# Optimization experiments

Measured on AMD Instinct MI355X. Metric: run time of the kernel, lower is better.

The kernel has to match this reference:

```python
import jax, jax.numpy as jnp
import numpy as np

N = 100000      # nodes (cells)
E = 1600000     # edges (kNN graph, avg degree 16)
DIM_IN = 128    # input features per cell
H = 8           # heads
C1 = 8          # per-head channels, layer 1 (concat -> 64)
DIM_OUT = 10    # classes (concat=False -> mean over heads)
NEG_SLOPE = 0.2


def setup_inputs() -> dict:
    key = jax.random.key(0)
    ks = jax.random.split(key, 10)
    s = 0.1
    return {
        "x": jax.random.normal(ks[0], (N, DIM_IN), dtype=jnp.float32),
        "edge_index": jax.random.randint(ks[1], (2, E), 0, N, dtype=jnp.int64),
        "W1": jax.random.normal(ks[2], (DIM_IN, H * C1), dtype=jnp.float32) * s,
        "a_src1": jax.random.normal(ks[3], (H, C1), dtype=jnp.float32) * s,
        "a_dst1": jax.random.normal(ks[4], (H, C1), dtype=jnp.float32) * s,
        "b1": jnp.zeros((H * C1,), dtype=jnp.float32),
        "W2": jax.random.normal(ks[5], (H * C1, H * DIM_OUT), dtype=jnp.float32) * s,
        "a_src2": jax.random.normal(ks[6], (H, DIM_OUT), dtype=jnp.float32) * s,
        "a_dst2": jax.random.normal(ks[7], (H, DIM_OUT), dtype=jnp.float32) * s,
        "b2": jnp.zeros((DIM_OUT,), dtype=jnp.float32),
    }


def _gat_layer(x, src, dst, W, a_src, a_dst, bias, concat, n):
    """PyG-style GATConv: gather -> edge attention -> segment softmax -> scatter."""
    h_, c_ = a_src.shape
    h = (x @ W).reshape(n, h_, c_)                       # [N, H, C]
    alpha_s = jnp.einsum('nhc,hc->nh', h, a_src)         # [N, H]
    alpha_d = jnp.einsum('nhc,hc->nh', h, a_dst)         # [N, H]
    # per-edge logits; PyG: message from src j to dst i, softmax over dst
    e = jax.nn.leaky_relu(alpha_s[src] + alpha_d[dst], NEG_SLOPE)  # [E, H]
    e_max = jax.ops.segment_max(e, dst, num_segments=n)            # [N, H]
    e = jnp.exp(e - e_max[dst])
    denom = jax.ops.segment_sum(e, dst, num_segments=n)            # [N, H]
    alpha = e / denom[dst]                                          # [E, H]
    msg = h[src] * alpha[:, :, None]                                # [E, H, C]
    out = jax.ops.segment_sum(msg, dst, num_segments=n)             # [N, H, C]
    out = out.reshape(n, h_ * c_) if concat else out.mean(axis=1)
    return out + bias


def reference(x, edge_index, W1, a_src1, a_dst1, b1, W2, a_src2, a_dst2, b2):
    n = x.shape[0]
    loops = jnp.arange(n, dtype=edge_index.dtype)
    src = jnp.concatenate([edge_index[0], loops])  # PyG adds self-loops by default
    dst = jnp.concatenate([edge_index[1], loops])
    h = _gat_layer(x, src, dst, W1, a_src1, a_dst1, b1, True, n)   # [N, 64]
    h = jax.nn.elu(h)
    h = _gat_layer(h, src, dst, W2, a_src2, a_dst2, b2, False, n)  # [N, dim_out]
    return jax.nn.log_softmax(h, axis=1)
```

## Files before the change

kernel.cpp:

```cpp
#include <hip/hip_runtime.h>
#include <hip/hip_bf16.h>
#include <cstdint>

#define CAP 64
#define SLICES 8
#define CHUNK_EDGES 2048

__device__ __forceinline__ float lrelu(float v) { return fmaxf(v, 0.2f * v); }

typedef float f32x2 __attribute__((ext_vector_type(2)));
__device__ __forceinline__ float2 q2f(unsigned short u) {
    f32x2 v = __builtin_amdgcn_cvt_pk_f32_fp8((int)u, false);
    return make_float2(v.x, v.y);
}
__device__ __forceinline__ int f2q4(float a, float b, float c, float d) {
    int p = __builtin_amdgcn_cvt_pk_fp8_f32(a, b, 0, false);
    p = __builtin_amdgcn_cvt_pk_fp8_f32(c, d, p, true);
    return p;
}
__device__ __forceinline__ float b2f(unsigned short u) { return __uint_as_float(((unsigned)u) << 16); }
__device__ __forceinline__ unsigned short f2b(float f) {
    unsigned u = __float_as_uint(f);
    return (unsigned short)((u + 0x7FFFu + ((u >> 16) & 1u)) >> 16);
}

__global__ __launch_bounds__(256, 4) void k_bg(const int* __restrict__ ei, int E, int N,
                                               int* __restrict__ cnt, int* __restrict__ bucket,
                                               const float* __restrict__ x,
                                               const float* __restrict__ W,
                                               const float* __restrict__ asrc,
                                               const float* __restrict__ adst,
                                               unsigned char* __restrict__ h1q,
                                               float* __restrict__ als, float* __restrict__ ald,
                                               int buildBlocks) {
    __shared__ unsigned short xs[64 * 132];
    if ((int)blockIdx.x < buildBlocks) {
        const int s = blockIdx.x & (SLICES - 1);
        const int chunk = blockIdx.x >> 3;
        const int sliceN = (N + SLICES - 1) / SLICES;
        const int lo = s * sliceN;
        const int hi = min(N, lo + sliceN);
        const int base = chunk * CHUNK_EDGES;
        if (base + CHUNK_EDGES <= E) {
            const int e0 = base + (int)threadIdx.x * 4;
            const int e1 = e0 + 1024;
            int4 d0 = *(const int4*)(ei + E + e0);
            int4 s0 = *(const int4*)(ei + e0);
            int4 d1 = *(const int4*)(ei + E + e1);
            int4 s1 = *(const int4*)(ei + e1);
            int a0 = -1, a1 = -1, a2 = -1, a3 = -1, a4 = -1, a5 = -1, a6 = -1, a7 = -1;
            if (d0.x >= lo && d0.x < hi) a0 = atomicAdd(&cnt[d0.x], 1);
            if (d0.y >= lo && d0.y < hi) a1 = atomicAdd(&cnt[d0.y], 1);
            if (d0.z >= lo && d0.z < hi) a2 = atomicAdd(&cnt[d0.z], 1);
            if (d0.w >= lo && d0.w < hi) a3 = atomicAdd(&cnt[d0.w], 1);
            if (d1.x >= lo && d1.x < hi) a4 = atomicAdd(&cnt[d1.x], 1);
            if (d1.y >= lo && d1.y < hi) a5 = atomicAdd(&cnt[d1.y], 1);
            if (d1.z >= lo && d1.z < hi) a6 = atomicAdd(&cnt[d1.z], 1);
            if (d1.w >= lo && d1.w < hi) a7 = atomicAdd(&cnt[d1.w], 1);
            if (a0 >= 0 && a0 < CAP) bucket[(size_t)d0.x * CAP + a0] = s0.x;
            if (a1 >= 0 && a1 < CAP) bucket[(size_t)d0.y * CAP + a1] = s0.y;
            if (a2 >= 0 && a2 < CAP) bucket[(size_t)d0.z * CAP + a2] = s0.z;
            if (a3 >= 0 && a3 < CAP) bucket[(size_t)d0.w * CAP + a3] = s0.w;
            if (a4 >= 0 && a4 < CAP) bucket[(size_t)d1.x * CAP + a4] = s1.x;
            if (a5 >= 0 && a5 < CAP) bucket[(size_t)d1.y * CAP + a5] = s1.y;
            if (a6 >= 0 && a6 < CAP) bucket[(size_t)d1.z * CAP + a6] = s1.z;
            if (a7 >= 0 && a7 < CAP) bucket[(size_t)d1.w * CAP + a7] = s1.w;
        } else {
            const int end = E;
            for (int e = base + (int)threadIdx.x; e < end; e += 256) {
                int d = ei[E + e];
                if (d >= lo && d < hi) {
                    int a = atomicAdd(&cnt[d], 1);
                    if (a < CAP) bucket[(size_t)d * CAP + a] = ei[e];
                }
            }
        }
        return;
    }
    const int t = threadIdx.x;
    const int rowBase = ((int)blockIdx.x - buildBlocks) * 64;
#pragma unroll
    for (int i = 0; i < 8; ++i) {
        int g = i * 256 + t;
        int r = g >> 5, c4 = (g & 31) << 2;
        float4 v = make_float4(0.f, 0.f, 0.f, 0.f);
        int row = rowBase + r;
        if (row < N) v = *(const float4*)(x + (size_t)row * 128 + c4);
        ushort4 u;
        u.x = f2b(v.x); u.y = f2b(v.y); u.z = f2b(v.z); u.w = f2b(v.w);
        *(ushort4*)(&xs[r * 132 + c4]) = u;
    }
    __syncthreads();
    const int tx = t & 15;
    const int ty = t >> 4;
    float acc[4][4] = {};
#pragma unroll 2
    for (int kc = 0; kc < 32; ++kc) {
        float a_[4][4];
#pragma unroll
        for (int i = 0; i < 4; ++i) {
            ushort4 u = *(const ushort4*)(&xs[(4 * ty + i) * 132 + kc * 4]);
            a_[i][0] = b2f(u.x); a_[i][1] = b2f(u.y); a_[i][2] = b2f(u.z); a_[i][3] = b2f(u.w);
        }
        float4 w[4];
#pragma unroll
        for (int kk = 0; kk < 4; ++kk) w[kk] = *(const float4*)(W + (size_t)(kc * 4 + kk) * 64 + tx * 4);
#pragma unroll
        for (int i = 0; i < 4; ++i) {
#pragma unroll
            for (int j = 0; j < 4; ++j) {
                acc[i][j] += a_[i][0] * ((const float*)&w[0])[j]
                           + a_[i][1] * ((const float*)&w[1])[j]
                           + a_[i][2] * ((const float*)&w[2])[j]
                           + a_[i][3] * ((const float*)&w[3])[j];
            }
        }
    }
    const int h = tx >> 1;
    float4 av = *(const float4*)(asrc + tx * 4);
    float4 dv = *(const float4*)(adst + tx * 4);
#pragma unroll
    for (int i = 0; i < 4; ++i) {
        int row = rowBase + 4 * ty + i;
        float ps = acc[i][0] * av.x + acc[i][1] * av.y + acc[i][2] * av.z + acc[i][3] * av.w;
        float pd = acc[i][0] * dv.x + acc[i][1] * dv.y + acc[i][2] * dv.z + acc[i][3] * dv.w;
        ps += __shfl_xor(ps, 1);
        pd += __shfl_xor(pd, 1);
        if (row < N) {
            *(int*)(h1q + (size_t)row * 64 + tx * 4) = f2q4(acc[i][0], acc[i][1], acc[i][2], acc[i][3]);
            if ((tx & 1) == 0) {
                als[(size_t)row * 8 + h] = ps;
                ald[(size_t)row * 8 + h] = pd;
            }
        }
    }
}

__global__ __launch_bounds__(256) void k_gemm2(const float* __restrict__ hin,
                                               const float* __restrict__ W,
                                               const float* __restrict__ asrc,
                                               const float* __restrict__ adst,
                                               unsigned char* __restrict__ h2q,
                                               float* __restrict__ ald, int N) {
    __shared__ float xs[64 * 68];
    __shared__ float wt[80 * 68];
    const int t = threadIdx.x;
    const int rowBase = blockIdx.x * 64;
#pragma unroll
    for (int i = 0; i < 4; ++i) {
        int g = i * 256 + t;
        int r = g >> 4, c4 = (g & 15) << 2;
        float4 v = make_float4(0.f, 0.f, 0.f, 0.f);
        int row = rowBase + r;
        if (row < N) v = *(const float4*)(hin + (size_t)row * 64 + c4);
        *(float4*)(&xs[r * 68 + c4]) = v;
    }
#pragma unroll
    for (int i = 0; i < 20; ++i) {
        int g = i * 256 + t;
        int k = g / 80, c = g % 80;
        wt[c * 68 + k] = W[g];
    }
    __syncthreads();
    const int tx = t & 15;
    const int ty = t >> 4;
    float acc[4][5] = {};
#pragma unroll 4
    for (int kc = 0; kc < 16; ++kc) {
        float4 a[4];
#pragma unroll
        for (int i = 0; i < 4; ++i) a[i] = *(const float4*)(&xs[(4 * ty + i) * 68 + kc * 4]);
        float4 w[5];
#pragma unroll
        for (int j = 0; j < 5; ++j) w[j] = *(const float4*)(&wt[(5 * tx + j) * 68 + kc * 4]);
#pragma unroll
        for (int i = 0; i < 4; ++i) {
#pragma unroll
            for (int j = 0; j < 5; ++j) {
                acc[i][j] += a[i].x * w[j].x + a[i].y * w[j].y + a[i].z * w[j].z + a[i].w * w[j].w;
            }
        }
    }
    const int h = tx >> 1;
    float a2[5], d2[5];
#pragma unroll
    for (int j = 0; j < 5; ++j) { a2[j] = asrc[tx * 5 + j]; d2[j] = adst[tx * 5 + j]; }
    __syncthreads();
    unsigned char* qs = (unsigned char*)xs;
#pragma unroll
    for (int i = 0; i < 4; ++i) {
        int row = rowBase + 4 * ty + i;
        float ps = 0.f, pd = 0.f;
#pragma unroll
        for (int j = 0; j < 5; ++j) { ps += acc[i][j] * a2[j]; pd += acc[i][j] * d2[j]; }
        ps += __shfl_xor(ps, 1);
        pd += __shfl_xor(pd, 1);
        int p0 = __builtin_amdgcn_cvt_pk_fp8_f32(acc[i][0], acc[i][1], 0, false);
        int p1 = __builtin_amdgcn_cvt_pk_fp8_f32(acc[i][2], acc[i][3], 0, false);
        int p2 = __builtin_amdgcn_cvt_pk_fp8_f32(acc[i][4], acc[i][4], 0, false);
        unsigned char* q = qs + (4 * ty + i) * 96 + h * 12 + (tx & 1) * 5;
        q[0] = (unsigned char)(p0 & 0xFF);
        q[1] = (unsigned char)((p0 >> 8) & 0xFF);
        q[2] = (unsigned char)(p1 & 0xFF);
        q[3] = (unsigned char)((p1 >> 8) & 0xFF);
        q[4] = (unsigned char)(p2 & 0xFF);
        if ((tx & 1) == 0) {
            *(unsigned short*)(qs + (size_t)(4 * ty + i) * 96 + h * 12 + 10) = f2b(ps);
            if (row < N) ald[(size_t)row * 8 + h] = pd;
        }
    }
    __syncthreads();
    for (int g = t; g < 1536; g += 256) {
        int row = g / 24;
        if (rowBase + row < N)
            *(unsigned int*)(h2q + (size_t)rowBase * 96 + (size_t)g * 4) = ((unsigned int*)qs)[g];
    }
}

__global__ __launch_bounds__(256) void k_agg1(const int* __restrict__ cnt, const int* __restrict__ bucket,
                                              const unsigned char* __restrict__ h1q,
                                              const float* __restrict__ als, const float* __restrict__ ald,
                                              const float* __restrict__ b1,
                                              float* __restrict__ helu, int N) {
    const int t = threadIdx.x;
    const int n = blockIdx.x * 32 + (t >> 3);
    const int h = t & 7;
    if (n >= N) return;
    float acc[8] = {};
    float den = 0.f;
    const float aldh = ald[(size_t)n * 8 + h];
    auto body = [&](int m0, int m1, float a_s, float val) {
        float wl = __expf(lrelu(a_s + aldh)) * val;
        den += wl;
        f32x2 v;
        v = __builtin_amdgcn_cvt_pk_f32_fp8(m0, false); acc[0] += wl * v.x; acc[1] += wl * v.y;
        v = __builtin_amdgcn_cvt_pk_f32_fp8(m0, true);  acc[2] += wl * v.x; acc[3] += wl * v.y;
        v = __builtin_amdgcn_cvt_pk_f32_fp8(m1, false); acc[4] += wl * v.x; acc[5] += wl * v.y;
        v = __builtin_amdgcn_cvt_pk_f32_fp8(m1, true);  acc[6] += wl * v.x; acc[7] += wl * v.y;
    };
    {
        const unsigned char* r = h1q + (size_t)n * 64 + h * 8;
        body(*(const int*)r, *(const int*)(r + 4), als[(size_t)n * 8 + h], 1.f);
    }
    const int k = min(cnt[n], CAP);
    const int* bp = bucket + (size_t)n * CAP;
    if (k > 0) {
        const int kg = ((k - 1) >> 2) << 2;
        int4 nxt = *(const int4*)(bp);
        for (int i0 = 0; i0 < k; i0 += 4) {
            int4 cur = nxt;
            nxt = *(const int4*)(bp + min(i0 + 4, kg));
            const int rem = k - i0;
            const int s0 = cur.x;
            const int s1 = (rem > 1) ? cur.y : cur.x;
            const int s2 = (rem > 2) ? cur.z : cur.x;
            const int s3 = (rem > 3) ? cur.w : cur.x;
            const int2 r0 = *(const int2*)(h1q + (size_t)s0 * 64 + h * 8);
            const int2 r1 = *(const int2*)(h1q + (size_t)s1 * 64 + h * 8);
            const int2 r2 = *(const int2*)(h1q + (size_t)s2 * 64 + h * 8);
            const int2 r3 = *(const int2*)(h1q + (size_t)s3 * 64 + h * 8);
            const float a0 = als[(size_t)s0 * 8 + h];
            const float a1 = als[(size_t)s1 * 8 + h];
            const float a2 = als[(size_t)s2 * 8 + h];
            const float a3 = als[(size_t)s3 * 8 + h];
            body(r0.x, r0.y, a0, 1.f);
            body(r1.x, r1.y, a1, (rem > 1) ? 1.f : 0.f);
            body(r2.x, r2.y, a2, (rem > 2) ? 1.f : 0.f);
            body(r3.x, r3.y, a3, (rem > 3) ? 1.f : 0.f);
        }
    }
    float inv = 1.f / den;
    float o[8];
#pragma unroll
    for (int j = 0; j < 8; ++j) {
        float v = acc[j] * inv + b1[h * 8 + j];
        o[j] = v > 0.f ? v : __expf(v) - 1.f;
    }
    *(float4*)(helu + (size_t)n * 64 + h * 8)     = make_float4(o[0], o[1], o[2], o[3]);
    *(float4*)(helu + (size_t)n * 64 + h * 8 + 4) = make_float4(o[4], o[5], o[6], o[7]);
}

__global__ __launch_bounds__(256) void k_agg2(const int* __restrict__ cnt, const int* __restrict__ bucket,
                                              const unsigned char* __restrict__ h2q,
                                              const float* __restrict__ ald,
                                              const float* __restrict__ b2,
                                              float* __restrict__ out, int N) {
    const int t = threadIdx.x;
    const int n = blockIdx.x * 32 + (t >> 3);
    const int h = t & 7;
    if (n >= N) return;
    float acc[10] = {};
    float den = 0.f;
    const float aldh = ald[(size_t)n * 8 + h];
    auto body = [&](int m0, int m1, int m2, float val) {
        float a_s = b2f((unsigned short)(((unsigned)m2) >> 16));
        float wl = __expf(lrelu(a_s + aldh)) * val;
        den += wl;
        f32x2 v;
        v = __builtin_amdgcn_cvt_pk_f32_fp8(m0, false); acc[0] += wl * v.x; acc[1] += wl * v.y;
        v = __builtin_amdgcn_cvt_pk_f32_fp8(m0, true);  acc[2] += wl * v.x; acc[3] += wl * v.y;
        v = __builtin_amdgcn_cvt_pk_f32_fp8(m1, false); acc[4] += wl * v.x; acc[5] += wl * v.y;
        v = __builtin_amdgcn_cvt_pk_f32_fp8(m1, true);  acc[6] += wl * v.x; acc[7] += wl * v.y;
        v = __builtin_amdgcn_cvt_pk_f32_fp8(m2, false); acc[8] += wl * v.x; acc[9] += wl * v.y;
    };
    {
        const unsigned char* r = h2q + (size_t)n * 96 + h * 12;
        body(*(const int*)r, *(const int*)(r + 4), *(const int*)(r + 8), 1.f);
    }
    const int k = min(cnt[n], CAP);
    const int* bp = bucket + (size_t)n * CAP;
    if (k > 0) {
        const int kg = ((k - 1) >> 2) << 2;
        int4 nxt = *(const int4*)(bp);
        for (int i0 = 0; i0 < k; i0 += 4) {
            int4 cur = nxt;
            nxt = *(const int4*)(bp + min(i0 + 4, kg));
            const int rem = k - i0;
            const int s0 = cur.x;
            const int s1 = (rem > 1) ? cur.y : cur.x;
            const int s2 = (rem > 2) ? cur.z : cur.x;
            const int s3 = (rem > 3) ? cur.w : cur.x;
            const unsigned char* p0 = h2q + (size_t)s0 * 96 + h * 12;
            const unsigned char* p1 = h2q + (size_t)s1 * 96 + h * 12;
            const unsigned char* p2 = h2q + (size_t)s2 * 96 + h * 12;
            const unsigned char* p3 = h2q + (size_t)s3 * 96 + h * 12;
            const int m00 = *(const int*)p0, m01 = *(const int*)(p0 + 4), m02 = *(const int*)(p0 + 8);
            const int m10 = *(const int*)p1, m11 = *(const int*)(p1 + 4), m12 = *(const int*)(p1 + 8);
            const int m20 = *(const int*)p2, m21 = *(const int*)(p2 + 4), m22 = *(const int*)(p2 + 8);
            const int m30 = *(const int*)p3, m31 = *(const int*)(p3 + 4), m32 = *(const int*)(p3 + 8);
            body(m00, m01, m02, 1.f);
            body(m10, m11, m12, (rem > 1) ? 1.f : 0.f);
            body(m20, m21, m22, (rem > 2) ? 1.f : 0.f);
            body(m30, m31, m32, (rem > 3) ? 1.f : 0.f);
        }
    }
    float inv = 1.f / den;
#pragma unroll
    for (int j = 0; j < 10; ++j) acc[j] *= inv;
#pragma unroll
    for (int off = 1; off < 8; off <<= 1) {
#pragma unroll
        for (int j = 0; j < 10; ++j) acc[j] += __shfl_xor(acc[j], off);
    }
    if (h == 0) {
        float m[10];
#pragma unroll
        for (int j = 0; j < 10; ++j) m[j] = acc[j] * 0.125f + b2[j];
        float mx = -1e30f;
#pragma unroll
        for (int j = 0; j < 10; ++j) mx = fmaxf(mx, m[j]);
        float ssum = 0.f;
#pragma unroll
        for (int j = 0; j < 10; ++j) ssum += __expf(m[j] - mx);
        float lg = __logf(ssum);
#pragma unroll
        for (int j = 0; j < 10; ++j) out[(size_t)n * 10 + j] = m[j] - mx - lg;
    }
}

extern "C" void kernel_launch(void* const* d_in, const int* in_sizes, int n_in,
                              void* d_out, int out_size, void* d_ws, size_t ws_size,
                              hipStream_t stream) {
    const float* x     = (const float*)d_in[0];
    const int*   ei    = (const int*)d_in[1];
    const float* W1    = (const float*)d_in[2];
    const float* asrc1 = (const float*)d_in[3];
    const float* adst1 = (const float*)d_in[4];
    const float* b1    = (const float*)d_in[5];
    const float* W2    = (const float*)d_in[6];
    const float* asrc2 = (const float*)d_in[7];
    const float* adst2 = (const float*)d_in[8];
    const float* b2    = (const float*)d_in[9];
    float* out = (float*)d_out;

    int N = in_sizes[0] / 128;
    int E = in_sizes[1] / 2;

    char* base = (char*)d_ws;
    size_t off = 0;
    auto alloc = [&](size_t bytes) {
        char* p = base + off;
        off = (off + bytes + 255) & ~(size_t)255;
        return p;
    };
    int*            cnt    = (int*)alloc((size_t)N * 4);
    int*            bucket = (int*)alloc((size_t)N * CAP * 4);
    float*          helu   = (float*)alloc((size_t)N * 64 * 4);
    unsigned char*  hq     = (unsigned char*)alloc((size_t)N * 96);
    float*          als    = (float*)alloc((size_t)N * 8 * 4);
    float*          ald    = (float*)alloc((size_t)N * 8 * 4);
    (void)ws_size; (void)n_in; (void)out_size;

    (void)hipMemsetAsync(cnt, 0, (size_t)N * 4, stream);
    int chunks = (E + CHUNK_EDGES - 1) / CHUNK_EDGES;
    int buildBlocks = chunks * SLICES;
    int gemmBlocks = (N + 63) / 64;
    k_bg<<<buildBlocks + gemmBlocks, 256, 0, stream>>>(ei, E, N, cnt, bucket,
                                                       x, W1, asrc1, adst1, hq, als, ald, buildBlocks);
    k_agg1<<<(N + 31) / 32, 256, 0, stream>>>(cnt, bucket, hq, als, ald, b1, helu, N);
    k_gemm2<<<(N + 63) / 64, 256, 0, stream>>>(helu, W2, asrc2, adst2, hq, ald, N);
    k_agg2<<<(N + 31) / 32, 256, 0, stream>>>(cnt, bucket, hq, ald, b2, out, N);
}
```

Measured before the change: 323.3 us.

## Fuse layer-1 aggregation into layer-2 GEMM via shared-memory staging

```diff
diff --git a/kernel.cpp b/kernel.cpp
--- a/kernel.cpp
+++ b/kernel.cpp
@@ -136,30 +136,96 @@
     }
 }
 
-__global__ __launch_bounds__(256) void k_gemm2(const float* __restrict__ hin,
-                                               const float* __restrict__ W,
-                                               const float* __restrict__ asrc,
-                                               const float* __restrict__ adst,
-                                               unsigned char* __restrict__ h2q,
-                                               float* __restrict__ ald, int N) {
+__global__ __launch_bounds__(256) void k_ag(const int* __restrict__ cnt, const int* __restrict__ bucket,
+                                            const unsigned char* __restrict__ h1q,
+                                            const float* __restrict__ als, const float* __restrict__ aldin,
+                                            const float* __restrict__ b1,
+                                            const float* __restrict__ W,
+                                            const float* __restrict__ asrc,
+                                            const float* __restrict__ adst,
+                                            unsigned char* __restrict__ h2q,
+                                            float* __restrict__ ald, int N) {
     __shared__ float xs[64 * 68];
     __shared__ float wt[80 * 68];
     const int t = threadIdx.x;
     const int rowBase = blockIdx.x * 64;
 #pragma unroll
-    for (int i = 0; i < 4; ++i) {
-        int g = i * 256 + t;
-        int r = g >> 4, c4 = (g & 15) << 2;
-        float4 v = make_float4(0.f, 0.f, 0.f, 0.f);
-        int row = rowBase + r;
-        if (row < N) v = *(const float4*)(hin + (size_t)row * 64 + c4);
-        *(float4*)(&xs[r * 68 + c4]) = v;
-    }
-#pragma unroll
     for (int i = 0; i < 20; ++i) {
         int g = i * 256 + t;
         int k = g / 80, c = g % 80;
         wt[c * 68 + k] = W[g];
+    }
+    {
+        const int n = rowBase + (t >> 2);
+        const int sub = t & 3;
+        if (n < N) {
+            float2 aldh = *(const float2*)(aldin + (size_t)n * 8 + sub * 2);
+            float acc[16] = {};
+            float den0 = 0.f, den1 = 0.f;
+            auto body = [&](int4 m, float2 a_s, float val) {
+                float wl0 = __expf(lrelu(a_s.x + aldh.x)) * val;
+                float wl1 = __expf(lrelu(a_s.y + aldh.y)) * val;
+                den0 += wl0; den1 += wl1;
+                f32x2 v;
+                v = __builtin_amdgcn_cvt_pk_f32_fp8(m.x, false); acc[0] += wl0 * v.x; acc[1] += wl0 * v.y;
+                v = __builtin_amdgcn_cvt_pk_f32_fp8(m.x, true);  acc[2] += wl0 * v.x; acc[3] += wl0 * v.y;
+                v = __builtin_amdgcn_cvt_pk_f32_fp8(m.y, false); acc[4] += wl0 * v.x; acc[5] += wl0 * v.y;
+                v = __builtin_amdgcn_cvt_pk_f32_fp8(m.y, true);  acc[6] += wl0 * v.x; acc[7] += wl0 * v.y;
+                v = __builtin_amdgcn_cvt_pk_f32_fp8(m.z, false); acc[8] += wl1 * v.x; acc[9] += wl1 * v.y;
+                v = __builtin_amdgcn_cvt_pk_f32_fp8(m.z, true);  acc[10] += wl1 * v.x; acc[11] += wl1 * v.y;
+                v = __builtin_amdgcn_cvt_pk_f32_fp8(m.w, false); acc[12] += wl1 * v.x; acc[13] += wl1 * v.y;
+                v = __builtin_amdgcn_cvt_pk_f32_fp8(m.w, true);  acc[14] += wl1 * v.x; acc[15] += wl1 * v.y;
+            };
+            {
+                body(*(const int4*)(h1q + (size_t)n * 64 + sub * 16),
+                     *(const float2*)(als + (size_t)n * 8 + sub * 2), 1.f);
+            }
+            const int k = min(cnt[n], CAP);
+            const int* bp = bucket + (size_t)n * CAP;
+            if (k > 0) {
+                const int kg = ((k - 1) >> 2) << 2;
+                int4 nxt = *(const int4*)(bp);
+                for (int i0 = 0; i0 < k; i0 += 4) {
+                    int4 cur = nxt;
+                    nxt = *(const int4*)(bp + min(i0 + 4, kg));
+                    const int rem = k - i0;
+                    const int s0 = cur.x;
+                    const int s1 = (rem > 1) ? cur.y : cur.x;
+                    const int s2 = (rem > 2) ? cur.z : cur.x;
+                    const int s3 = (rem > 3) ? cur.w : cur.x;
+                    const int4 r0 = *(const int4*)(h1q + (size_t)s0 * 64 + sub * 16);
+                    const int4 r1 = *(const int4*)(h1q + (size_t)s1 * 64 + sub * 16);
+                    const int4 r2 = *(const int4*)(h1q + (size_t)s2 * 64 + sub * 16);
+                    const int4 r3 = *(const int4*)(h1q + (size_t)s3 * 64 + sub * 16);
+                    const float2 a0 = *(const float2*)(als + (size_t)s0 * 8 + sub * 2);
+                    const float2 a1 = *(const float2*)(als + (size_t)s1 * 8 + sub * 2);
+                    const float2 a2 = *(const float2*)(als + (size_t)s2 * 8 + sub * 2);
+                    const float2 a3 = *(const float2*)(als + (size_t)s3 * 8 + sub * 2);
+                    body(r0, a0, 1.f);
+                    body(r1, a1, (rem > 1) ? 1.f : 0.f);
+                    body(r2, a2, (rem > 2) ? 1.f : 0.f);
+                    body(r3, a3, (rem > 3) ? 1.f : 0.f);
+                }
+            }
+            float inv0 = 1.f / den0, inv1 = 1.f / den1;
+            const float* bb = b1 + sub * 16;
+            float o[16];
+#pragma unroll
+            for (int j = 0; j < 8; ++j) {
+                float v = acc[j] * inv0 + bb[j];
+                o[j] = v > 0.f ? v : __expf(v) - 1.f;
+            }
+#pragma unroll
+            for (int j = 8; j < 16; ++j) {
+                float v = acc[j] * inv1 + bb[j];
+                o[j] = v > 0.f ? v : __expf(v) - 1.f;
+            }
+            float* dst = &xs[(t >> 2) * 68 + sub * 16];
+            *(float4*)(dst)      = make_float4(o[0],  o[1],  o[2],  o[3]);
+            *(float4*)(dst + 4)  = make_float4(o[4],  o[5],  o[6],  o[7]);
+            *(float4*)(dst + 8)  = make_float4(o[8],  o[9],  o[10], o[11]);
+            *(float4*)(dst + 12) = make_float4(o[12], o[13], o[14], o[15]);
+        }
     }
     __syncthreads();
     const int tx = t & 15;
@@ -215,69 +281,6 @@
         if (rowBase + row < N)
             *(unsigned int*)(h2q + (size_t)rowBase * 96 + (size_t)g * 4) = ((unsigned int*)qs)[g];
     }
-}
-
-__global__ __launch_bounds__(256) void k_agg1(const int* __restrict__ cnt, const int* __restrict__ bucket,
-                                              const unsigned char* __restrict__ h1q,
-                                              const float* __restrict__ als, const float* __restrict__ ald,
-                                              const float* __restrict__ b1,
-                                              float* __restrict__ helu, int N) {
-    const int t = threadIdx.x;
-    const int n = blockIdx.x * 32 + (t >> 3);
-    const int h = t & 7;
-    if (n >= N) return;
-    float acc[8] = {};
-    float den = 0.f;
-    const float aldh = ald[(size_t)n * 8 + h];
-    auto body = [&](int m0, int m1, float a_s, float val) {
-        float wl = __expf(lrelu(a_s + aldh)) * val;
-        den += wl;
-        f32x2 v;
-        v = __builtin_amdgcn_cvt_pk_f32_fp8(m0, false); acc[0] += wl * v.x; acc[1] += wl * v.y;
-        v = __builtin_amdgcn_cvt_pk_f32_fp8(m0, true);  acc[2] += wl * v.x; acc[3] += wl * v.y;
-        v = __builtin_amdgcn_cvt_pk_f32_fp8(m1, false); acc[4] += wl * v.x; acc[5] += wl * v.y;
-        v = __builtin_amdgcn_cvt_pk_f32_fp8(m1, true);  acc[6] += wl * v.x; acc[7] += wl * v.y;
-    };
-    {
-        const unsigned char* r = h1q + (size_t)n * 64 + h * 8;
-        body(*(const int*)r, *(const int*)(r + 4), als[(size_t)n * 8 + h], 1.f);
-    }
-    const int k = min(cnt[n], CAP);
-    const int* bp = bucket + (size_t)n * CAP;
-    if (k > 0) {
-        const int kg = ((k - 1) >> 2) << 2;
-        int4 nxt = *(const int4*)(bp);
-        for (int i0 = 0; i0 < k; i0 += 4) {
-            int4 cur = nxt;
-            nxt = *(const int4*)(bp + min(i0 + 4, kg));
-            const int rem = k - i0;
-            const int s0 = cur.x;
-            const int s1 = (rem > 1) ? cur.y : cur.x;
-            const int s2 = (rem > 2) ? cur.z : cur.x;
-            const int s3 = (rem > 3) ? cur.w : cur.x;
-            const int2 r0 = *(const int2*)(h1q + (size_t)s0 * 64 + h * 8);
-            const int2 r1 = *(const int2*)(h1q + (size_t)s1 * 64 + h * 8);
-            const int2 r2 = *(const int2*)(h1q + (size_t)s2 * 64 + h * 8);
-            const int2 r3 = *(const int2*)(h1q + (size_t)s3 * 64 + h * 8);
-            const float a0 = als[(size_t)s0 * 8 + h];
-            const float a1 = als[(size_t)s1 * 8 + h];
-            const float a2 = als[(size_t)s2 * 8 + h];
-            const float a3 = als[(size_t)s3 * 8 + h];
-            body(r0.x, r0.y, a0, 1.f);
-            body(r1.x, r1.y, a1, (rem > 1) ? 1.f : 0.f);
-            body(r2.x, r2.y, a2, (rem > 2) ? 1.f : 0.f);
-            body(r3.x, r3.y, a3, (rem > 3) ? 1.f : 0.f);
-        }
-    }
-    float inv = 1.f / den;
-    float o[8];
-#pragma unroll
-    for (int j = 0; j < 8; ++j) {
-        float v = acc[j] * inv + b1[h * 8 + j];
-        o[j] = v > 0.f ? v : __expf(v) - 1.f;
-    }
-    *(float4*)(helu + (size_t)n * 64 + h * 8)     = make_float4(o[0], o[1], o[2], o[3]);
-    *(float4*)(helu + (size_t)n * 64 + h * 8 + 4) = make_float4(o[4], o[5], o[6], o[7]);
 }
 
 __global__ __launch_bounds__(256) void k_agg2(const int* __restrict__ cnt, const int* __restrict__ bucket,
@@ -385,8 +388,8 @@
     };
     int*            cnt    = (int*)alloc((size_t)N * 4);
     int*            bucket = (int*)alloc((size_t)N * CAP * 4);
-    float*          helu   = (float*)alloc((size_t)N * 64 * 4);
-    unsigned char*  hq     = (unsigned char*)alloc((size_t)N * 96);
+    unsigned char*  h1q    = (unsigned char*)alloc((size_t)N * 64);
+    unsigned char*  h2q    = (unsigned char*)alloc((size_t)N * 96);
     float*          als    = (float*)alloc((size_t)N * 8 * 4);
     float*          ald    = (float*)alloc((size_t)N * 8 * 4);
     (void)ws_size; (void)n_in; (void)out_size;
@@ -396,8 +399,8 @@
     int buildBlocks = chunks * SLICES;
     int gemmBlocks = (N + 63) / 64;
     k_bg<<<buildBlocks + gemmBlocks, 256, 0, stream>>>(ei, E, N, cnt, bucket,
-                                                       x, W1, asrc1, adst1, hq, als, ald, buildBlocks);
-    k_agg1<<<(N + 31) / 32, 256, 0, stream>>>(cnt, bucket, hq, als, ald, b1, helu, N);
-    k_gemm2<<<(N + 63) / 64, 256, 0, stream>>>(helu, W2, asrc2, adst2, hq, ald, N);
-    k_agg2<<<(N + 31) / 32, 256, 0, stream>>>(cnt, bucket, hq, ald, b2, out, N);
-}
+                                                       x, W1, asrc1, adst1, h1q, als, ald, buildBlocks);
+    k_ag<<<(N + 63) / 64, 256, 0, stream>>>(cnt, bucket, h1q, als, ald, b1,
+                                            W2, asrc2, adst2, h2q, ald, N);
+    k_agg2<<<(N + 31) / 32, 256, 0, stream>>>(cnt, bucket, h2q, ald, b2, out, N);
+}
```

New measurement: 313.9 us. -2.9%, faster.
